# Kernel optimization log

Hardware: AMD Instinct MI355X
Metric: run time of the kernel (lower is better)

The kernel has to match this reference:

```python
import jax, jax.numpy as jnp
import numpy as np

SIZE = 8192
DIM = 256
N = 32768
BETA = 0.25
DECAY = 0.99
EPS = 1e-5


def setup_inputs() -> dict:
    key = jax.random.key(0)
    kz, ke = jax.random.split(key)
    z = jax.random.normal(kz, (N, DIM), dtype=jnp.float32)
    # init = randn * 0.1, ema_embed_sum initialized as a clone of embeddings
    embeddings = jax.random.normal(ke, (SIZE, DIM), dtype=jnp.float32) * 0.1
    ema_embed_sum = embeddings
    ema_cluster_size = jnp.zeros((SIZE,), dtype=jnp.float32)
    usage_counter = jnp.zeros((SIZE,), dtype=jnp.int64)
    return {
        "z": z,
        "embeddings": embeddings,
        "ema_cluster_size": ema_cluster_size,
        "ema_embed_sum": ema_embed_sum,
        "usage_counter": usage_counter,
    }


def reference(z, embeddings, ema_cluster_size, ema_embed_sum, usage_counter):
    # Squared euclidean distances; argmin is identical to cdist argmin.
    z2 = jnp.sum(z * z, axis=-1, keepdims=True)              # [N, 1]
    e2 = jnp.sum(embeddings * embeddings, axis=-1)           # [K]
    d2 = z2 - 2.0 * jnp.matmul(z, embeddings.T) + e2         # [N, K]
    indices = jnp.argmin(d2, axis=-1)                         # [N]

    quantized = embeddings[indices]                           # [N, D] gather

    # usage_counter: vectorized equivalent of the per-index python loop
    counts_f = jax.ops.segment_sum(
        jnp.ones((z.shape[0],), dtype=jnp.float32), indices, num_segments=SIZE
    )                                                         # [K] == onehot.sum(0)
    new_usage = usage_counter + counts_f.astype(usage_counter.dtype)

    sg = jax.lax.stop_gradient
    commit_loss = BETA * jnp.mean((z - sg(quantized)) ** 2)
    codebook_loss = jnp.mean((quantized - sg(z)) ** 2)
    loss = commit_loss + codebook_loss

    # EMA update (training mode), all under no-grad semantics
    embed_sum = jax.ops.segment_sum(z, indices, num_segments=SIZE)  # onehot.T @ z
    new_cluster_size = DECAY * ema_cluster_size + (1.0 - DECAY) * counts_f
    new_embed_sum = DECAY * ema_embed_sum + (1.0 - DECAY) * embed_sum
    n = jnp.sum(new_cluster_size)
    cluster = (new_cluster_size + EPS) / (n + SIZE * EPS) * n
    new_embeddings = new_embed_sum / cluster[:, None]

    # straight-through estimator
    quantized_st = z + sg(quantized - z)
    return (indices, quantized_st, loss, new_embeddings, new_cluster_size,
            new_embed_sum, new_usage)
```

## Files before the change

kernel.cpp:

```cpp
#include <hip/hip_runtime.h>

#define NZ 32768
#define KE 8192
#define DD 256
#define NCHUNK 4
#define CH (KE / NCHUNK)
#define NSLICE (NCHUNK * 2)
#define ITERS ((CH / 128) * 8)
#define THR_GAP 0.05f
#define BIASF 128.0f

typedef __attribute__((ext_vector_type(8))) _Float16 f16x8;
typedef __attribute__((ext_vector_type(4))) float f32x4;
typedef unsigned int uint32;


__device__ __forceinline__ float wave_reduce_sum(float v) {
#pragma unroll
  for (int m = 32; m >= 1; m >>= 1) v += __shfl_xor(v, m, 64);
  return v;
}

__global__ void prep_kernel(const float* __restrict__ emb, unsigned short* __restrict__ e_dst,
                            float* __restrict__ e_sq, const float* __restrict__ z,
                            unsigned short* __restrict__ z_dst, float* __restrict__ z_sq,
                            const float* __restrict__ ema_cs, float* __restrict__ sema_out,
                            float* __restrict__ o_loss) {
  const int gb = blockIdx.x;
  if (gb < (KE / 4) + (NZ / 4)) {
    const float* src;
    unsigned short* dst;
    float* sq;
    int row;
    if (gb < KE / 4) {
      src = emb; dst = e_dst; sq = e_sq;
      row = gb * 4 + (threadIdx.x >> 6);
    } else {
      src = z; dst = z_dst; sq = z_sq;
      row = (gb - KE / 4) * 4 + (threadIdx.x >> 6);
    }
    const int lane = threadIdx.x & 63;
    const float4 v = *reinterpret_cast<const float4*>(src + (size_t)row * DD + lane * 4);
    alignas(8) _Float16 hv[4] = {(_Float16)v.x, (_Float16)v.y, (_Float16)v.z, (_Float16)v.w};
    *reinterpret_cast<uint2*>(dst + (size_t)row * DD + lane * 4) =
        *reinterpret_cast<const uint2*>(hv);
    float s = (v.x * v.x + v.y * v.y) + (v.z * v.z + v.w * v.w);
    s = wave_reduce_sum(s);
    if (lane == 0) sq[row] = s;
  } else {
    __shared__ float red[256];
    float s = 0.f;
    for (int i = threadIdx.x; i < KE; i += 256) s += ema_cs[i];
    red[threadIdx.x] = s;
    __syncthreads();
    for (int off = 128; off >= 1; off >>= 1) {
      if (threadIdx.x < off) red[threadIdx.x] += red[threadIdx.x + off];
      __syncthreads();
    }
    if (threadIdx.x == 0) {
      sema_out[0] = red[0];
      o_loss[0] = 0.f;
    }
  }
}


#define LSTR 32

#define LOADB(RS, itv)                                                          \
  if ((itv) < ITERS) {                                                          \
    const int kb_ = ((itv) & 7) * 32;                                           \
    const size_t bo_ = (size_t)((itv) >> 3) * 128 * DD + kb_;                   \
    RS##b0 = *reinterpret_cast<const uint4*>(ef + boff0 + bo_);                 \
    RS##b1 = *reinterpret_cast<const uint4*>(ef + boff1 + bo_);                 \
  }

#define WRITEB(buf, RS)                                                         \
  *reinterpret_cast<uint4*>(&ldsB[buf][ur][usw]) = RS##b0;                      \
  *reinterpret_cast<uint4*>(&ldsB[buf][ur + 64][usw]) = RS##b1;

__launch_bounds__(256, 2)
__global__ void mfma_argmin_kernel(const unsigned short* __restrict__ zf,
                                   const unsigned short* __restrict__ ef,
                                   const float* __restrict__ e2,
                                   float4* __restrict__ pt) {
  __shared__ unsigned short ldsA[8][64][LSTR];
  __shared__ unsigned short ldsB[4][128][LSTR];
  const int bid = blockIdx.x;
  const int c = (bid & 7) >> 1;
  const int mblk = ((bid >> 3) << 1) | (bid & 1);
  const int row0 = mblk * 64;
  const int cbase = c * CH;
  const int tid = threadIdx.x;
  const int wid = tid >> 6, lane = tid & 63;
  const int wr = wid >> 1, wc = wid & 1;
  const int lg = lane >> 4, l15 = lane & 15;

  const int ur = tid >> 2;
  const int usw = (((tid & 3) ^ ((ur >> 1) & 3)) << 3);
  const int csw = ((lg ^ ((l15 >> 1) & 3)) << 3);
  const size_t aoff0 = (size_t)(row0 + ur) * DD + (tid & 3) * 8;
  const size_t boff0 = (size_t)(cbase + ur) * DD + (tid & 3) * 8;
  const size_t boff1 = boff0 + (size_t)64 * DD;

  uint32 k1[2][4], k2[2][4];
#pragma unroll
  for (int i = 0; i < 2; ++i)
#pragma unroll
    for (int r = 0; r < 4; ++r) { k1[i][r] = 0xFFFFFFFFu; k2[i][r] = 0xFFFFFFFFu; }

  f32x4 acc[2][4];

  uint4 p0_b0, p0_b1, p1_b0, p1_b1;

#pragma unroll
  for (int ki = 0; ki < 8; ++ki) {
    const uint4 va0 = *reinterpret_cast<const uint4*>(zf + aoff0 + ki * 32);
    *reinterpret_cast<uint4*>(&ldsA[ki][ur][usw]) = va0;
  }
  LOADB(p0_, 0)
  WRITEB(0, p0_)
  LOADB(p1_, 1)
  WRITEB(1, p1_)
  LOADB(p0_, 2)
  LOADB(p1_, 3)
  __syncthreads();

#define COMPUTE(buf, itv)                                                               \
  {                                                                                     \
    const int ki_ = (itv) & 7;                                                          \
    if (ki_ == 0) {                                                                     \
      _Pragma("unroll") for (int i = 0; i < 2; ++i)                                     \
          _Pragma("unroll") for (int j = 0; j < 4; ++j) acc[i][j] = (f32x4)(0.f);       \
    }                                                                                   \
    f16x8 ah[2], bh[4];                                                                 \
    _Pragma("unroll") for (int x = 0; x < 2; ++x)                                       \
      ah[x] = *reinterpret_cast<const f16x8*>(&ldsA[ki_][wr * 32 + x * 16 + l15][csw]); \
    _Pragma("unroll") for (int x = 0; x < 4; ++x)                                       \
      bh[x] = *reinterpret_cast<const f16x8*>(&ldsB[buf][wc * 64 + x * 16 + l15][csw]); \
    _Pragma("unroll") for (int i = 0; i < 2; ++i)                                       \
        _Pragma("unroll") for (int j = 0; j < 4; ++j)                                   \
            acc[i][j] = __builtin_amdgcn_mfma_f32_16x16x32_f16(ah[i], bh[j], acc[i][j], 0, 0, 0); \
    if (ki_ == 7) {                                                                     \
      const int col0 = cbase + ((itv) >> 3) * 128;                                      \
      const uint32 tb_ = (uint32)(((itv) >> 3) << 2);                                   \
      _Pragma("unroll") for (int j = 0; j < 4; ++j) {                                   \
        const int code = col0 + wc * 64 + j * 16 + l15;                                 \
        const float e2b = e2[code] + BIASF;                                             \
        const uint32 meta = tb_ | (uint32)j;                                            \
        _Pragma("unroll") for (int i = 0; i < 2; ++i)                                   \
            _Pragma("unroll") for (int r = 0; r < 4; ++r) {                             \
          const float vb = fmaf(-2.f, acc[i][j][r], e2b);                               \
          const uint32 key = (__float_as_uint(vb) & 0xFFFFFFC0u) | meta;                \
          if (key < k1[i][r]) {                                                         \
            k2[i][r] = k1[i][r];                                                        \
            k1[i][r] = key;                                                             \
          } else if (key < k2[i][r]) {                                                  \
            k2[i][r] = key;                                                             \
          }                                                                             \
        }                                                                               \
      }                                                                                 \
    }                                                                                   \
  }

  for (int it = 0; it < ITERS; it += 4) {
    WRITEB(2, p0_)
    LOADB(p0_, it + 4)
    COMPUTE(0, it)
    WRITEB(3, p1_)
    LOADB(p1_, it + 5)
    COMPUTE(1, it + 1)
    __syncthreads();
    WRITEB(0, p0_)
    LOADB(p0_, it + 6)
    COMPUTE(2, it + 2)
    WRITEB(1, p1_)
    LOADB(p1_, it + 7)
    COMPUTE(3, it + 3)
    __syncthreads();
  }

  float bv1[2][4], bv2[2][4];
  uint32 bpi[2][4];
  const uint32 cb_ = (uint32)(cbase + wc * 64 + l15);
#pragma unroll
  for (int i = 0; i < 2; ++i)
#pragma unroll
    for (int r = 0; r < 4; ++r) {
      const uint32 a1 = k1[i][r], a2 = k2[i][r];
      bv1[i][r] = __uint_as_float(a1 & 0xFFFFFFC0u) - BIASF;
      bv2[i][r] = __uint_as_float(a2 & 0xFFFFFFC0u) - BIASF;
      const uint32 c1 = cb_ + ((a1 & 60u) >> 2) * 128u + ((a1 & 3u) << 4);
      const uint32 c2 = cb_ + ((a2 & 60u) >> 2) * 128u + ((a2 & 3u) << 4);
      bpi[i][r] = c1 | (c2 << 16);
    }

#pragma unroll
  for (int m = 1; m <= 8; m <<= 1) {
#pragma unroll
    for (int i = 0; i < 2; ++i)
#pragma unroll
      for (int r = 0; r < 4; ++r) {
        const float ov1 = __shfl_xor(bv1[i][r], m, 64);
        const float ov2 = __shfl_xor(bv2[i][r], m, 64);
        const uint32 op = (uint32)__shfl_xor((int)bpi[i][r], m, 64);
        const uint32 ai1 = bpi[i][r] & 0xFFFFu, oi1 = op & 0xFFFFu;
        const bool ol = (ov1 < bv1[i][r]) || (ov1 == bv1[i][r] && oi1 < ai1);
        const float w1 = ol ? ov1 : bv1[i][r];
        const uint32 wi1 = ol ? oi1 : ai1;
        const float w2 = ol ? ov2 : bv2[i][r];
        const uint32 wi2 = ol ? (op >> 16) : (bpi[i][r] >> 16);
        const float l1 = ol ? bv1[i][r] : ov1;
        const uint32 li1 = ol ? ai1 : oi1;
        const bool s2 = (l1 < w2) || (l1 == w2 && li1 < wi2);
        bv1[i][r] = w1;
        bv2[i][r] = s2 ? l1 : w2;
        bpi[i][r] = wi1 | ((s2 ? li1 : wi2) << 16);
      }
  }
  if (l15 == 0) {
    const int slice = c * 2 + wc;
#pragma unroll
    for (int i = 0; i < 2; ++i)
#pragma unroll
      for (int r = 0; r < 4; ++r) {
        const int row = row0 + wr * 32 + i * 16 + lg * 4 + r;
        pt[(size_t)slice * NZ + row] =
            make_float4(bv1[i][r], bv2[i][r], __uint_as_float(bpi[i][r]), 0.f);
      }
  }
}

__global__ void combine_kernel(const float* __restrict__ z, const float* __restrict__ emb,
                               const float* __restrict__ z2, const float* __restrict__ e2,
                               const float4* __restrict__ pt, float* __restrict__ oidx_f,
                               int* __restrict__ oidx_i, float* __restrict__ oq,
                               float* __restrict__ oloss) {
  const int row = blockIdx.x * 4 + (threadIdx.x >> 6);
  const int lane = threadIdx.x & 63;
  const int wid = threadIdx.x >> 6;
  const float4 p = pt[(size_t)(lane & 7) * NZ + row];
  const float v1 = p.x, v2 = p.y;
  const uint32 pk = __float_as_uint(p.z);
  float m = v1;
#pragma unroll
  for (int s = 1; s <= 4; s <<= 1) m = fminf(m, __shfl_xor(m, s, 64));

  const float4 zv = *reinterpret_cast<const float4*>(z + (size_t)row * DD + lane * 4);
  const float z2r = z2[row];
  float bestd = 3.4e38f;
  int besti = KE;
#pragma unroll 1
  for (int cnum = 0; cnum < 16; ++cnum) {
    const int src = (lane & 56) | (cnum >> 1);
    const float vc = __shfl((cnum & 1) ? v2 : v1, src, 64);
    const uint32 pkc = (uint32)__shfl((int)pk, src, 64);
    const int idxc = (cnum & 1) ? (int)(pkc >> 16) : (int)(pkc & 0xFFFFu);
    if (vc < m + THR_GAP) {
      const float4 ev = *reinterpret_cast<const float4*>(emb + (size_t)idxc * DD + lane * 4);
      float s = (zv.x * ev.x + zv.y * ev.y) + (zv.z * ev.z + zv.w * ev.w);
      s = wave_reduce_sum(s);
      const float d = (z2r - 2.f * s) + e2[idxc];
      if (d < bestd || (d == bestd && idxc < besti)) { bestd = d; besti = idxc; }
    }
  }
  if (lane == 0) {
    oidx_f[row] = (float)besti;
    oidx_i[row] = besti;
  }
  const float4 qv = *reinterpret_cast<const float4*>(emb + (size_t)besti * DD + lane * 4);
  *reinterpret_cast<float4*>(oq + (size_t)row * DD + lane * 4) = qv;
  const float dx = zv.x - qv.x, dy = zv.y - qv.y, dz = zv.z - qv.z, dw = zv.w - qv.w;
  float s = (dx * dx + dy * dy) + (dz * dz + dw * dw);
  s = wave_reduce_sum(s);
  __shared__ float red[4];
  if (lane == 0) red[wid] = s;
  __syncthreads();
  if (threadIdx.x == 0) {
    const float t = (red[0] + red[1]) + (red[2] + red[3]);
    atomicAdd(oloss, t * (1.25f / ((float)NZ * (float)DD)));
  }
}

__global__ void perk_kernel(const float* __restrict__ z, const float* __restrict__ ema_cs,
                            const float* __restrict__ ema_es, const int* __restrict__ usage,
                            const int* __restrict__ idx, const float* __restrict__ sema,
                            float* __restrict__ o_emb, float* __restrict__ o_cs,
                            float* __restrict__ o_es, float* __restrict__ o_us) {
  const int k0 = blockIdx.x * 8;
  const int tid = threadIdx.x;
  __shared__ int cnt;
  __shared__ int cnt8[8];
  __shared__ int stot[8];
  __shared__ int rows[2048];
  float acc[8];
#pragma unroll
  for (int q = 0; q < 8; ++q) acc[q] = 0.f;
  if (tid < 8) stot[tid] = 0;
  for (int base = 0; base < NZ; base += 2048) {
    if (tid == 0) cnt = 0;
    if (tid < 8) cnt8[tid] = 0;
    __syncthreads();
#pragma unroll
    for (int t = 0; t < 2048; t += 256) {
      const int r = base + t + tid;
      const int q = idx[r] - k0;
      if ((unsigned)q < 8u) {
        rows[atomicAdd(&cnt, 1)] = (r << 3) | q;
        atomicAdd(&cnt8[q], 1);
      }
    }
    __syncthreads();
    const int cq = cnt;
    if (tid < 8) stot[tid] += cnt8[tid];
    for (int m = 0; m < cq; ++m) {
      const int rr = rows[m];
      const float v = z[(size_t)(rr >> 3) * DD + tid];
      const int q = rr & 7;
#pragma unroll
      for (int qq = 0; qq < 8; ++qq)
        if (qq == q) acc[qq] += v;
    }
    __syncthreads();
  }
  const float n = 0.99f * sema[0] + 0.01f * (float)NZ;
  const float dn = n + (float)KE * 1e-5f;
#pragma unroll
  for (int q = 0; q < 8; ++q) {
    const float ncs = 0.99f * ema_cs[k0 + q] + 0.01f * (float)stot[q];
    const float nes = 0.99f * ema_es[(size_t)(k0 + q) * DD + tid] + 0.01f * acc[q];
    o_es[(size_t)(k0 + q) * DD + tid] = nes;
    o_emb[(size_t)(k0 + q) * DD + tid] = nes / ((ncs + 1e-5f) / dn * n);
  }
  if (tid < 8) {
    o_cs[k0 + tid] = 0.99f * ema_cs[k0 + tid] + 0.01f * (float)stot[tid];
    o_us[k0 + tid] = (float)(usage[k0 + tid] + stot[tid]);
  }
}


extern "C" void kernel_launch(void* const* d_in, const int* in_sizes, int n_in,
                              void* d_out, int out_size, void* d_ws, size_t ws_size,
                              hipStream_t stream) {
  const float* z = (const float*)d_in[0];
  const float* emb = (const float*)d_in[1];
  const float* ema_cs = (const float*)d_in[2];
  const float* ema_es = (const float*)d_in[3];
  const int* usage = (const int*)d_in[4];

  float* out = (float*)d_out;
  float* o_idx = out;
  float* o_q = o_idx + NZ;
  float* o_loss = o_q + (size_t)NZ * DD;
  float* o_emb = o_loss + 1;
  float* o_cs = o_emb + (size_t)KE * DD;
  float* o_es = o_cs + KE;
  float* o_us = o_es + (size_t)KE * DD;

  char* w = (char*)d_ws;
  size_t off = 0;
  auto alloc = [&](size_t bytes) -> char* {
    char* r = w + off;
    off = (off + bytes + 255) & ~(size_t)255;
    return r;
  };
  float* ws_e2 = (float*)alloc(KE * 4);
  float* ws_z2 = (float*)alloc(NZ * 4);
  float* ws_sema = (float*)alloc(256);
  int* ws_idx = (int*)alloc(NZ * 4);
  float4* ws_pt = (float4*)alloc((size_t)NSLICE * NZ * 16);
  unsigned short* z_f16 = (unsigned short*)alloc((size_t)NZ * DD * 2);
  unsigned short* e_f16 = (unsigned short*)alloc((size_t)KE * DD * 2);
  (void)ws_size;

  prep_kernel<<<(KE / 4) + (NZ / 4) + 1, 256, 0, stream>>>(emb, e_f16, ws_e2, z, z_f16,
                                                           ws_z2, ema_cs, ws_sema, o_loss);

  mfma_argmin_kernel<<<(NZ / 64) * NCHUNK, 256, 0, stream>>>(z_f16, e_f16, ws_e2, ws_pt);
  combine_kernel<<<NZ / 4, 256, 0, stream>>>(z, emb, ws_z2, ws_e2, ws_pt, o_idx, ws_idx,
                                             o_q, o_loss);
  perk_kernel<<<KE / 8, 256, 0, stream>>>(z, ema_cs, ema_es, usage, ws_idx, ws_sema,
                                          o_emb, o_cs, o_es, o_us);
}
```

Baseline: 386.6 us.

## Keep A fragments in registers and deepen B LDS pipeline to eight stages

The z tile's fp16 fragments are now loaded once from LDS into registers (areg) and reused for every codebook tile, so the per-iteration A loads from LDS go away. The LDS space that held A is reused as four extra B buffers, giving eight B stages with four register prefetch sets. That halves the number of __syncthreads per K-slice. The cost is much higher VGPR pressure (64 extra regs for areg plus 8 uint4 prefetch registers), which may hurt occupancy under launch_bounds(256,2) or cause spills.

Result: faster. 365.9 us (-5.4%).

```diff
diff --git a/kernel.cpp b/kernel.cpp
--- a/kernel.cpp
+++ b/kernel.cpp
@@ -67,6 +67,8 @@
 
 #define LSTR 32
 
+#define LDSA(ki, r) (&ldsB[4 + ((ki) >> 1)][(((ki) & 1) << 6) + (r)][0])
+
 #define LOADB(RS, itv)                                                          \
   if ((itv) < ITERS) {                                                          \
     const int kb_ = ((itv) & 7) * 32;                                           \
@@ -84,8 +86,7 @@
                                    const unsigned short* __restrict__ ef,
                                    const float* __restrict__ e2,
                                    float4* __restrict__ pt) {
-  __shared__ unsigned short ldsA[8][64][LSTR];
-  __shared__ unsigned short ldsB[4][128][LSTR];
+  __shared__ unsigned short ldsB[8][128][LSTR];
   const int bid = blockIdx.x;
   const int c = (bid & 7) >> 1;
   const int mblk = ((bid >> 3) << 1) | (bid & 1);
@@ -110,20 +111,34 @@
     for (int r = 0; r < 4; ++r) { k1[i][r] = 0xFFFFFFFFu; k2[i][r] = 0xFFFFFFFFu; }
 
   f32x4 acc[2][4];
-
-  uint4 p0_b0, p0_b1, p1_b0, p1_b1;
-
+  f16x8 areg[8][2];
+
+  uint4 q0_b0, q0_b1, q1_b0, q1_b1, q2_b0, q2_b1, q3_b0, q3_b1;
+
+  LOADB(q0_, 0)
+  LOADB(q1_, 1)
+  LOADB(q2_, 2)
+  LOADB(q3_, 3)
 #pragma unroll
   for (int ki = 0; ki < 8; ++ki) {
     const uint4 va0 = *reinterpret_cast<const uint4*>(zf + aoff0 + ki * 32);
-    *reinterpret_cast<uint4*>(&ldsA[ki][ur][usw]) = va0;
-  }
-  LOADB(p0_, 0)
-  WRITEB(0, p0_)
-  LOADB(p1_, 1)
-  WRITEB(1, p1_)
-  LOADB(p0_, 2)
-  LOADB(p1_, 3)
+    *reinterpret_cast<uint4*>(LDSA(ki, ur) + usw) = va0;
+  }
+  __syncthreads();
+#pragma unroll
+  for (int ki = 0; ki < 8; ++ki)
+#pragma unroll
+    for (int x = 0; x < 2; ++x)
+      areg[ki][x] =
+          *reinterpret_cast<const f16x8*>(LDSA(ki, wr * 32 + x * 16 + l15) + csw);
+  WRITEB(0, q0_)
+  WRITEB(1, q1_)
+  WRITEB(2, q2_)
+  WRITEB(3, q3_)
+  LOADB(q0_, 4)
+  LOADB(q1_, 5)
+  LOADB(q2_, 6)
+  LOADB(q3_, 7)
   __syncthreads();
 
 #define COMPUTE(buf, itv)                                                               \
@@ -133,14 +148,12 @@
       _Pragma("unroll") for (int i = 0; i < 2; ++i)                                     \
           _Pragma("unroll") for (int j = 0; j < 4; ++j) acc[i][j] = (f32x4)(0.f);       \
     }                                                                                   \
-    f16x8 ah[2], bh[4];                                                                 \
-    _Pragma("unroll") for (int x = 0; x < 2; ++x)                                       \
-      ah[x] = *reinterpret_cast<const f16x8*>(&ldsA[ki_][wr * 32 + x * 16 + l15][csw]); \
+    f16x8 bh[4];                                                                        \
     _Pragma("unroll") for (int x = 0; x < 4; ++x)                                       \
       bh[x] = *reinterpret_cast<const f16x8*>(&ldsB[buf][wc * 64 + x * 16 + l15][csw]); \
     _Pragma("unroll") for (int i = 0; i < 2; ++i)                                       \
         _Pragma("unroll") for (int j = 0; j < 4; ++j)                                   \
-            acc[i][j] = __builtin_amdgcn_mfma_f32_16x16x32_f16(ah[i], bh[j], acc[i][j], 0, 0, 0); \
+            acc[i][j] = __builtin_amdgcn_mfma_f32_16x16x32_f16(areg[ki_][i], bh[j], acc[i][j], 0, 0, 0); \
     if (ki_ == 7) {                                                                     \
       const int col0 = cbase + ((itv) >> 3) * 128;                                      \
       const uint32 tb_ = (uint32)(((itv) >> 3) << 2);                                   \
@@ -163,20 +176,32 @@
     }                                                                                   \
   }
 
-  for (int it = 0; it < ITERS; it += 4) {
-    WRITEB(2, p0_)
-    LOADB(p0_, it + 4)
+  for (int it = 0; it < ITERS; it += 8) {
+    WRITEB(4, q0_)
+    LOADB(q0_, it + 8)
     COMPUTE(0, it)
-    WRITEB(3, p1_)
-    LOADB(p1_, it + 5)
+    WRITEB(5, q1_)
+    LOADB(q1_, it + 9)
     COMPUTE(1, it + 1)
-    __syncthreads();
-    WRITEB(0, p0_)
-    LOADB(p0_, it + 6)
+    WRITEB(6, q2_)
+    LOADB(q2_, it + 10)
     COMPUTE(2, it + 2)
-    WRITEB(1, p1_)
-    LOADB(p1_, it + 7)
+    WRITEB(7, q3_)
+    LOADB(q3_, it + 11)
     COMPUTE(3, it + 3)
+    __syncthreads();
+    WRITEB(0, q0_)
+    LOADB(q0_, it + 12)
+    COMPUTE(4, it + 4)
+    WRITEB(1, q1_)
+    LOADB(q1_, it + 13)
+    COMPUTE(5, it + 5)
+    WRITEB(2, q2_)
+    LOADB(q2_, it + 14)
+    COMPUTE(6, it + 6)
+    WRITEB(3, q3_)
+    LOADB(q3_, it + 15)
+    COMPUTE(7, it + 7)
     __syncthreads();
   }
 
```
